# Optimization experiments

Hardware: AMD Instinct MI355X
Metric: run time of the kernel (lower is better)

## Reference

```python
import jax, jax.numpy as jnp
import numpy as np
import math

B, T, D = 2, 2048, 2048
H, DH = 16, 128
DKV, DQ, DR = 512, 1024, 64
ROPE_BASE = 500000.0
EPS = 1e-6
SCALE = 1.0 / math.sqrt(DH + DR)


def setup_inputs() -> dict:
    key = jax.random.key(0)
    ks = jax.random.split(key, 12)
    s = 0.02
    return {
        'x': jax.random.normal(ks[0], (B, T, D), jnp.float32),
        'W_DQ': jax.random.normal(ks[1], (D, DQ), jnp.float32) * s,
        'W_UQ': jax.random.normal(ks[2], (DQ, H * DH), jnp.float32) * s,
        'W_QR': jax.random.normal(ks[3], (DQ, H * DR), jnp.float32) * s,
        'W_DKV': jax.random.normal(ks[4], (D, DKV), jnp.float32) * s,
        'W_UK': jax.random.normal(ks[5], (DKV, H * DH), jnp.float32) * s,
        'W_UV': jax.random.normal(ks[6], (DKV, H * DH), jnp.float32) * s,
        'W_KR': jax.random.normal(ks[7], (D, DR), jnp.float32) * s,
        'W_O': jax.random.normal(ks[8], (H * DH, D), jnp.float32) * s,
        'q_norm_w': jnp.ones((DQ,), jnp.float32),
        'kv_norm_w': jnp.ones((DKV,), jnp.float32),
    }


def _rmsnorm(v, w):
    n = jax.lax.rsqrt(jnp.mean(v * v, axis=-1, keepdims=True) + EPS)
    return v * n * w


def _rotate_half(v):
    v1, v2 = jnp.split(v, 2, axis=-1)
    return jnp.concatenate([-v2, v1], axis=-1)


def _rope_tables(seq_len):
    inv_freq = 1.0 / (ROPE_BASE ** (jnp.arange(0, DR, 2, dtype=jnp.float32) / DR))
    t = jnp.arange(seq_len, dtype=jnp.float32)
    freqs = jnp.outer(t, inv_freq)              # (S, DR/2)
    emb = jnp.concatenate([freqs, freqs], -1)   # (S, DR)
    return jnp.cos(emb), jnp.sin(emb)


def reference(x, W_DQ, W_UQ, W_QR, W_DKV, W_UK, W_UV, W_KR, W_O, q_norm_w, kv_norm_w):
    # Query path: low-rank compress -> RMSNorm -> up-project (content + rope parts)
    c_Q = _rmsnorm(x @ W_DQ, q_norm_w)                               # (B,T,DQ)
    q_C = (c_Q @ W_UQ).reshape(B, T, H, DH).transpose(0, 2, 1, 3)    # (B,H,T,DH)
    q_R = (c_Q @ W_QR).reshape(B, T, H, DR).transpose(0, 2, 1, 3)    # (B,H,T,DR)
    # KV path: joint low-rank latent + decoupled rope key
    c_KV = _rmsnorm(x @ W_DKV, kv_norm_w)                            # (B,T,DKV)
    k_C = (c_KV @ W_UK).reshape(B, T, H, DH).transpose(0, 2, 1, 3)   # (B,H,T,DH)
    v_C = (c_KV @ W_UV).reshape(B, T, H, DH).transpose(0, 2, 1, 3)   # (B,H,T,DH)
    k_R = (x @ W_KR)[:, None, :, :]                                  # (B,1,T,DR) shared across heads
    # Decoupled RoPE
    cos, sin = _rope_tables(T)
    cos = cos[None, None]; sin = sin[None, None]                     # (1,1,T,DR)
    q_R = q_R * cos + _rotate_half(q_R) * sin
    k_R = k_R * cos + _rotate_half(k_R) * sin
    k_R = jnp.broadcast_to(k_R, (B, H, T, DR))
    q = jnp.concatenate([q_C, q_R], axis=-1)                         # (B,H,T,DH+DR)
    k = jnp.concatenate([k_C, k_R], axis=-1)
    # Causal attention with MLA scale 1/sqrt(d_head + d_rope)
    scores = jnp.einsum('bhqd,bhkd->bhqk', q, k) * SCALE
    causal = jnp.tril(jnp.ones((T, T), bool))
    scores = jnp.where(causal, scores, jnp.finfo(scores.dtype).min)
    attn = jax.nn.softmax(scores, axis=-1)
    out = jnp.einsum('bhqk,bhkd->bhqd', attn, v_C)                   # (B,H,T,DH)
    out = out.transpose(0, 2, 1, 3).reshape(B, T, H * DH)
    return out @ W_O                                                 # (B,T,D)
```

## Files before the change

kernel.cpp:

```cpp
#include <hip/hip_runtime.h>
#include <cstdint>
#include <cstddef>

#define B_   2
#define T_   2048
#define D_   2048
#define H_   16
#define DH_  128
#define DQ_  1024
#define DKV_ 512
#define DR_  64
#define M_   4096
#define SCALE_ 0.07216878364870323f
#define SC2_   0.10412808709930322f
#define LN_BASE_ 13.122363377404328f

typedef unsigned short u16;
typedef __attribute__((ext_vector_type(8))) short short8;
typedef __attribute__((ext_vector_type(4))) float f32x4;

__device__ __forceinline__ float b2f(u16 u) { return __uint_as_float(((uint32_t)u) << 16); }
__device__ __forceinline__ u16 f2b(float f) {
    uint32_t x = __float_as_uint(f);
    return (u16)((x + 0x7fffu + ((x >> 16) & 1u)) >> 16);
}
__device__ __forceinline__ u16 f2b_fast(float f) {
    return (u16)((__float_as_uint(f) + 0x8000u) >> 16);
}

struct TPack {
    const float* src[8];
    u16*         dst[8];
    int K[8];
    int N[8];
    int ntx[8];
    int start[9];
};

__global__ __launch_bounds__(256) void prep_k(TPack p, const float* __restrict__ x,
                                              u16* __restrict__ xb, int ntr) {
    const int bid = blockIdx.x;
    if (bid < ntr) {
        __shared__ float tile[32][33];
        int w = 0;
#pragma unroll
        for (int i = 1; i < 8; ++i) if (bid >= p.start[i]) w = i;
        const int lt = bid - p.start[w];
        const int bx = lt % p.ntx[w], by = lt / p.ntx[w];
        const float* in = p.src[w];
        u16* out = p.dst[w];
        const int K = p.K[w], N = p.N[w];
        const int k0 = by * 32, n0 = bx * 32;
        const int tx = threadIdx.x & 31, ty = threadIdx.x >> 5;
#pragma unroll
        for (int i = 0; i < 4; ++i) {
            int k = k0 + ty + i * 8;
            int n = n0 + tx;
            tile[ty + i * 8][tx] = (n < N) ? in[(size_t)k * N + n] : 0.f;
        }
        __syncthreads();
#pragma unroll
        for (int i = 0; i < 4; ++i) {
            int n = n0 + ty + i * 8;
            out[(size_t)n * K + k0 + tx] = f2b(tile[tx][ty + i * 8]);
        }
    } else {
        const int i = ((bid - ntr) * 256 + threadIdx.x) * 4;
        const float4 v = *(const float4*)(x + i);
        ushort4 o;
        o.x = f2b(v.x); o.y = f2b(v.y); o.z = f2b(v.z); o.w = f2b(v.w);
        *(ushort4*)(xb + i) = o;
    }
}

template <int OUT_BF16>
__global__ __launch_bounds__(256) void gemm_tn(const u16* __restrict__ A,
                                               const u16* __restrict__ Bt,
                                               void* __restrict__ Cv,
                                               int N, int K) {
    __shared__ __attribute__((aligned(16))) u16 lA[128 * 32];
    __shared__ __attribute__((aligned(16))) u16 lB[128 * 32];
    const int m0 = blockIdx.y * 128, n0 = blockIdx.x * 128;
    const int tid = threadIdx.x, wave = tid >> 6, lane = tid & 63;
    const int wm = (wave >> 1) * 64, wn = (wave & 1) * 64;
    const int r = lane & 15, kq = lane >> 4;

    f32x4 acc[4][4];
#pragma unroll
    for (int i = 0; i < 4; ++i)
#pragma unroll
        for (int j = 0; j < 4; ++j) acc[i][j] = (f32x4){0.f, 0.f, 0.f, 0.f};

    for (int kk = 0; kk < K; kk += 32) {
#pragma unroll
        for (int p = 0; p < 2; ++p) {
            const int c = p * 256 + wave * 64 + lane;
            const u16* ga = A  + (size_t)(m0 + (c >> 2)) * K + kk + (c & 3) * 8;
            const u16* gb = Bt + (size_t)(n0 + (c >> 2)) * K + kk + (c & 3) * 8;
            u16* la = lA + (size_t)(p * 256 + wave * 64) * 8;
            u16* lb = lB + (size_t)(p * 256 + wave * 64) * 8;
            __builtin_amdgcn_global_load_lds(
                (const __attribute__((address_space(1))) uint32_t*)(uintptr_t)ga,
                (__attribute__((address_space(3))) uint32_t*)(uintptr_t)la, 16, 0, 0);
            __builtin_amdgcn_global_load_lds(
                (const __attribute__((address_space(1))) uint32_t*)(uintptr_t)gb,
                (__attribute__((address_space(3))) uint32_t*)(uintptr_t)lb, 16, 0, 0);
        }
        __syncthreads();
        short8 av[4], bv[4];
#pragma unroll
        for (int mi = 0; mi < 4; ++mi)
            av[mi] = *(const short8*)&lA[(wm + mi * 16 + r) * 32 + kq * 8];
#pragma unroll
        for (int ni = 0; ni < 4; ++ni)
            bv[ni] = *(const short8*)&lB[(wn + ni * 16 + r) * 32 + kq * 8];
#pragma unroll
        for (int mi = 0; mi < 4; ++mi)
#pragma unroll
            for (int ni = 0; ni < 4; ++ni)
                acc[mi][ni] = __builtin_amdgcn_mfma_f32_16x16x32_bf16(
                    av[mi], bv[ni], acc[mi][ni], 0, 0, 0);
        __syncthreads();
    }
    const int r4 = (lane >> 4) * 4, cc = lane & 15;
#pragma unroll
    for (int mi = 0; mi < 4; ++mi)
#pragma unroll
        for (int ni = 0; ni < 4; ++ni)
#pragma unroll
            for (int i = 0; i < 4; ++i) {
                const int row = m0 + wm + mi * 16 + r4 + i;
                const int col = n0 + wn + ni * 16 + cc;
                const float v = acc[mi][ni][i];
                if (OUT_BF16) ((u16*)Cv)[(size_t)row * N + col] = f2b(v);
                else          ((float*)Cv)[(size_t)row * N + col] = v;
            }
}

__global__ __launch_bounds__(256) void gemm_pair(const u16* __restrict__ A0,
                                                 const u16* __restrict__ B0,
                                                 u16* __restrict__ C0, int N0, int K0,
                                                 const u16* __restrict__ A1,
                                                 const u16* __restrict__ B1,
                                                 u16* __restrict__ C1, int N1, int K1,
                                                 int nx0) {
    __shared__ __attribute__((aligned(16))) u16 lA[128 * 32];
    __shared__ __attribute__((aligned(16))) u16 lB[128 * 32];
    const int sel = (int)blockIdx.x >= nx0;
    const u16* A  = sel ? A1 : A0;
    const u16* Bt = sel ? B1 : B0;
    u16* Cv = sel ? C1 : C0;
    const int N = sel ? N1 : N0, K = sel ? K1 : K0;
    const int bx = sel ? (blockIdx.x - nx0) : blockIdx.x;
    const int m0 = blockIdx.y * 128, n0 = bx * 128;
    const int tid = threadIdx.x, wave = tid >> 6, lane = tid & 63;
    const int wm = (wave >> 1) * 64, wn = (wave & 1) * 64;
    const int r = lane & 15, kq = lane >> 4;

    f32x4 acc[4][4];
#pragma unroll
    for (int i = 0; i < 4; ++i)
#pragma unroll
        for (int j = 0; j < 4; ++j) acc[i][j] = (f32x4){0.f, 0.f, 0.f, 0.f};

    for (int kk = 0; kk < K; kk += 32) {
#pragma unroll
        for (int p = 0; p < 2; ++p) {
            const int c = p * 256 + wave * 64 + lane;
            const u16* ga = A  + (size_t)(m0 + (c >> 2)) * K + kk + (c & 3) * 8;
            const u16* gb = Bt + (size_t)(n0 + (c >> 2)) * K + kk + (c & 3) * 8;
            u16* la = lA + (size_t)(p * 256 + wave * 64) * 8;
            u16* lb = lB + (size_t)(p * 256 + wave * 64) * 8;
            __builtin_amdgcn_global_load_lds(
                (const __attribute__((address_space(1))) uint32_t*)(uintptr_t)ga,
                (__attribute__((address_space(3))) uint32_t*)(uintptr_t)la, 16, 0, 0);
            __builtin_amdgcn_global_load_lds(
                (const __attribute__((address_space(1))) uint32_t*)(uintptr_t)gb,
                (__attribute__((address_space(3))) uint32_t*)(uintptr_t)lb, 16, 0, 0);
        }
        __syncthreads();
        short8 av[4], bv[4];
#pragma unroll
        for (int mi = 0; mi < 4; ++mi)
            av[mi] = *(const short8*)&lA[(wm + mi * 16 + r) * 32 + kq * 8];
#pragma unroll
        for (int ni = 0; ni < 4; ++ni)
            bv[ni] = *(const short8*)&lB[(wn + ni * 16 + r) * 32 + kq * 8];
#pragma unroll
        for (int mi = 0; mi < 4; ++mi)
#pragma unroll
            for (int ni = 0; ni < 4; ++ni)
                acc[mi][ni] = __builtin_amdgcn_mfma_f32_16x16x32_bf16(
                    av[mi], bv[ni], acc[mi][ni], 0, 0, 0);
        __syncthreads();
    }
    const int r4 = (lane >> 4) * 4, cc = lane & 15;
#pragma unroll
    for (int mi = 0; mi < 4; ++mi)
#pragma unroll
        for (int ni = 0; ni < 4; ++ni)
#pragma unroll
            for (int i = 0; i < 4; ++i) {
                const int row = m0 + wm + mi * 16 + r4 + i;
                const int col = n0 + wn + ni * 16 + cc;
                Cv[(size_t)row * N + col] = f2b(acc[mi][ni][i]);
            }
}

__global__ __launch_bounds__(256) void normrope_k(const u16* __restrict__ P1,
                                                  const float* __restrict__ qnw,
                                                  const float* __restrict__ kvnw,
                                                  u16* __restrict__ cQb,
                                                  u16* __restrict__ cKVb,
                                                  u16* __restrict__ kRb) {
    const int row = blockIdx.x;
    const int which = blockIdx.y;
    if (which < 2) {
        const int N = which ? 512 : 1024;
        const int off = which ? 1024 : 0;
        const float* w = which ? kvnw : qnw;
        u16* outp = which ? cKVb : cQb;
        const u16* src = P1 + (size_t)row * 1664 + off;
        const int j = threadIdx.x * 4;
        float v[4] = {0.f, 0.f, 0.f, 0.f};
        if (j < N) {
            ushort4 u = *(const ushort4*)(src + j);
            v[0] = b2f(u.x); v[1] = b2f(u.y); v[2] = b2f(u.z); v[3] = b2f(u.w);
        }
        float ss = v[0]*v[0] + v[1]*v[1] + v[2]*v[2] + v[3]*v[3];
#pragma unroll
        for (int offc = 32; offc; offc >>= 1) ss += __shfl_down(ss, offc);
        __shared__ float red[4];
        const int wave = threadIdx.x >> 6, lane = threadIdx.x & 63;
        if (lane == 0) red[wave] = ss;
        __syncthreads();
        const float tot = red[0] + red[1] + red[2] + red[3];
        const float sc = rsqrtf(tot / (float)N + 1e-6f);
        if (j < N) {
            ushort4 o;
            o.x = f2b(v[0] * sc * w[j]);
            o.y = f2b(v[1] * sc * w[j + 1]);
            o.z = f2b(v[2] * sc * w[j + 2]);
            o.w = f2b(v[3] * sc * w[j + 3]);
            *(ushort4*)(outp + (size_t)row * N + j) = o;
        }
    } else {
        const int j = threadIdx.x;
        if (j < 64) {
            const int t = row & (T_ - 1);
            const int i = j & 31;
            const float invf = __expf(-LN_BASE_ * (float)(2 * i) * (1.0f / 64.0f));
            const float ang = (float)t * invf;
            const float c = cosf(ang), s = sinf(ang);
            const u16* src = P1 + (size_t)row * 1664 + 1536;
            const float v = b2f(src[j]);
            const float rot = (j < 32) ? -b2f(src[j + 32]) : b2f(src[j - 32]);
            kRb[(size_t)row * 64 + j] = f2b(v * c + rot * s);
        }
    }
}

__global__ __launch_bounds__(256) void epilog2_k(const u16* __restrict__ P2,
                                                 u16* __restrict__ qRb,
                                                 const u16* __restrict__ P3,
                                                 u16* __restrict__ Vt) {
    const int bid = blockIdx.x;
    if (bid < 2048) {
        const int row = bid * 2 + (threadIdx.x >> 7);
        const int t = row & (T_ - 1);
        const int e0 = (threadIdx.x & 127) * 8;
        const u16* src = P2 + (size_t)row * 3072 + 2048;
        const int j0 = e0 & 63;
        const ushort4* pv = (const ushort4*)(src + e0);
        const ushort4* pr = (const ushort4*)(src + (j0 < 32 ? e0 + 32 : e0 - 32));
        const float sgn = (j0 < 32) ? -1.f : 1.f;
        ushort4 v01 = pv[0], v23 = pv[1];
        ushort4 r01 = pr[0], r23 = pr[1];
        const u16 vv[8] = {v01.x, v01.y, v01.z, v01.w, v23.x, v23.y, v23.z, v23.w};
        const u16 rr[8] = {r01.x, r01.y, r01.z, r01.w, r23.x, r23.y, r23.z, r23.w};
        u16 o[8];
#pragma unroll
        for (int k = 0; k < 8; ++k) {
            const int i = (j0 + k) & 31;
            const float invf = __expf(-LN_BASE_ * (float)(2 * i) * (1.0f / 64.0f));
            const float ang = (float)t * invf;
            o[k] = f2b(b2f(vv[k]) * cosf(ang) + sgn * b2f(rr[k]) * sinf(ang));
        }
        *(uint4*)(qRb + (size_t)row * 1024 + e0) = *(uint4*)o;
    } else {
        __shared__ u16 tile[64][72];
        const int tt = bid - 2048;
        const int b = tt >> 10;
        const int rem = tt & 1023;
        const int by = rem >> 5, bx = rem & 31;
        const int t0 = by * 64, c0 = bx * 64;
        const int tid = threadIdx.x;
        const int rr2 = tid >> 3;
        const int c8 = tid & 7;
#pragma unroll
        for (int p = 0; p < 2; ++p) {
            const int row = p * 32 + rr2;
            *(uint4*)&tile[row][c8 * 8] =
                *(const uint4*)(P3 + (size_t)(b * T_ + t0 + row) * 4096 + 2048 + c0 + c8 * 8);
        }
        __syncthreads();
#pragma unroll
        for (int p = 0; p < 2; ++p) {
            const int c = p * 32 + rr2;
            u16 tmp[8];
#pragma unroll
            for (int j = 0; j < 8; ++j) tmp[j] = tile[c8 * 8 + j][c];
            *(uint4*)(Vt + ((size_t)b * 2048 + c0 + c) * 2048 + t0 + c8 * 8) = *(uint4*)tmp;
        }
    }
}

#define ABQ  128
#define ABK  64
#define KSTR 200
#define VSTR 72
#define PSTR 72
#define QSTRIDE 3072
#define KSTRIDE 4096

__global__ __launch_bounds__(256, 2) void attn_mfma_k(
    const u16* __restrict__ qC, const u16* __restrict__ qR,
    const u16* __restrict__ kC, const u16* __restrict__ kR,
    const u16* __restrict__ Vt, u16* __restrict__ outp)
{
    __shared__ __attribute__((aligned(16))) u16 sK[64 * KSTR];
    __shared__ __attribute__((aligned(16))) u16 sV[128 * VSTR];
    __shared__ __attribute__((aligned(16))) u16 sP[4 * 32 * PSTR];

    const int h = blockIdx.y, b = blockIdx.z;
    const int qb = b ? (15 - blockIdx.x) : blockIdx.x;
    const int q0 = qb * ABQ;
    const int tid = threadIdx.x, wave = tid >> 6, lane = tid & 63;
    const int r = lane & 15, kq = lane >> 4, r4 = kq * 4;
    const int wq = wave * 32;

    short8 qf[2][6];
#pragma unroll
    for (int mt = 0; mt < 2; ++mt) {
        const int t = q0 + wq + mt * 16 + r;
        const u16* qcrow = qC + (size_t)(b * T_ + t) * QSTRIDE + h * 128 + kq * 8;
        const u16* qrrow = qR + (size_t)(b * T_ + t) * 1024 + h * 64 + kq * 8;
#pragma unroll
        for (int kc = 0; kc < 4; ++kc) qf[mt][kc] = *(const short8*)(qcrow + kc * 32);
#pragma unroll
        for (int kc = 0; kc < 2; ++kc) qf[mt][4 + kc] = *(const short8*)(qrrow + kc * 32);
    }

    f32x4 Oa[2][8];
#pragma unroll
    for (int mt = 0; mt < 2; ++mt)
#pragma unroll
        for (int nt = 0; nt < 8; ++nt) Oa[mt][nt] = (f32x4){0.f, 0.f, 0.f, 0.f};
    float Lrow[2][4] = {{0.f,0.f,0.f,0.f},{0.f,0.f,0.f,0.f}};

    u16* myP = sP + wave * 32 * PSTR;

    const int nkt = 2 * qb + 2;
    for (int kt = 0; kt < nkt; ++kt) {
        const int k0 = kt * ABK;
        for (int i = wave; i < 25; i += 4) {
            const int s = i * 64 + lane;
            const int rr = s / 25;
            int cc = s - rr * 25;
            if (cc > 23) cc = 0;
            const int t = k0 + rr;
            const u16* src = (cc < 16)
                ? kC + (size_t)(b * T_ + t) * KSTRIDE + h * 128 + cc * 8
                : kR + (size_t)(b * T_ + t) * 64 + (cc - 16) * 8;
            __builtin_amdgcn_global_load_lds(
                (const __attribute__((address_space(1))) uint32_t*)(uintptr_t)src,
                (__attribute__((address_space(3))) uint32_t*)(uintptr_t)(sK + i * 512),
                16, 0, 0);
        }
        for (int i = wave; i < 18; i += 4) {
            const int s = i * 64 + lane;
            const int rr = s / 9;
            int cc = s - rr * 9;
            if (cc > 7) cc = 0;
            const u16* src = Vt + ((size_t)(b * H_ + h) * 128 + rr) * T_ + k0 + cc * 8;
            __builtin_amdgcn_global_load_lds(
                (const __attribute__((address_space(1))) uint32_t*)(uintptr_t)src,
                (__attribute__((address_space(3))) uint32_t*)(uintptr_t)(sV + i * 512),
                16, 0, 0);
        }
        __syncthreads();

        f32x4 Sa[2][4];
#pragma unroll
        for (int mt = 0; mt < 2; ++mt)
#pragma unroll
            for (int nt = 0; nt < 4; ++nt) Sa[mt][nt] = (f32x4){0.f, 0.f, 0.f, 0.f};
#pragma unroll
        for (int kc = 0; kc < 6; ++kc) {
            short8 kf[4];
#pragma unroll
            for (int nt = 0; nt < 4; ++nt)
                kf[nt] = *(const short8*)&sK[(nt * 16 + r) * KSTR + (kc * 4 + kq) * 8];
#pragma unroll
            for (int mt = 0; mt < 2; ++mt)
#pragma unroll
                for (int nt = 0; nt < 4; ++nt)
                    Sa[mt][nt] = __builtin_amdgcn_mfma_f32_16x16x32_bf16(
                        qf[mt][kc], kf[nt], Sa[mt][nt], 0, 0, 0);
        }

        if (kt < nkt - 2) {
#pragma unroll
            for (int mt = 0; mt < 2; ++mt)
#pragma unroll
                for (int i = 0; i < 4; ++i) {
                    float sm = 0.f;
                    float p[4];
#pragma unroll
                    for (int nt = 0; nt < 4; ++nt) {
                        p[nt] = exp2f(Sa[mt][nt][i] * SC2_);
                        sm += p[nt];
                    }
                    Lrow[mt][i] += sm;
#pragma unroll
                    for (int nt = 0; nt < 4; ++nt)
                        myP[(mt * 16 + r4 + i) * PSTR + nt * 16 + r] = f2b_fast(p[nt]);
                }
        } else {
#pragma unroll
            for (int mt = 0; mt < 2; ++mt)
#pragma unroll
                for (int i = 0; i < 4; ++i) {
                    const int grow = q0 + wq + mt * 16 + r4 + i;
                    float sm = 0.f;
                    float p[4];
#pragma unroll
                    for (int nt = 0; nt < 4; ++nt) {
                        float pv = exp2f(Sa[mt][nt][i] * SC2_);
                        p[nt] = (k0 + nt * 16 + r > grow) ? 0.f : pv;
                        sm += p[nt];
                    }
                    Lrow[mt][i] += sm;
#pragma unroll
                    for (int nt = 0; nt < 4; ++nt)
                        myP[(mt * 16 + r4 + i) * PSTR + nt * 16 + r] = f2b_fast(p[nt]);
                }
        }

#pragma unroll
        for (int kc2 = 0; kc2 < 2; ++kc2) {
            short8 pf[2];
#pragma unroll
            for (int mt = 0; mt < 2; ++mt)
                pf[mt] = *(const short8*)&myP[(mt * 16 + r) * PSTR + (kc2 * 4 + kq) * 8];
#pragma unroll
            for (int nt = 0; nt < 8; ++nt) {
                const short8 vf = *(const short8*)&sV[(nt * 16 + r) * VSTR + (kc2 * 4 + kq) * 8];
#pragma unroll
                for (int mt = 0; mt < 2; ++mt)
                    Oa[mt][nt] = __builtin_amdgcn_mfma_f32_16x16x32_bf16(
                        pf[mt], vf, Oa[mt][nt], 0, 0, 0);
            }
        }
        __syncthreads();
    }

#pragma unroll
    for (int mt = 0; mt < 2; ++mt)
#pragma unroll
        for (int i = 0; i < 4; ++i) {
            float L = Lrow[mt][i];
            L += __shfl_xor(L, 1);
            L += __shfl_xor(L, 2);
            L += __shfl_xor(L, 4);
            L += __shfl_xor(L, 8);
            const float inv = 1.0f / L;
            const int t = q0 + wq + mt * 16 + r4 + i;
            u16* orow = outp + (size_t)(b * T_ + t) * 2048 + h * 128;
#pragma unroll
            for (int nt = 0; nt < 8; ++nt)
                orow[nt * 16 + r] = f2b(Oa[mt][nt][i] * inv);
        }
}

extern "C" void kernel_launch(void* const* d_in, const int* in_sizes, int n_in,
                              void* d_out, int out_size, void* d_ws, size_t ws_size,
                              hipStream_t stream) {
    (void)in_sizes; (void)n_in; (void)out_size; (void)ws_size;
    const float* x     = (const float*)d_in[0];
    const float* W_DQ  = (const float*)d_in[1];
    const float* W_UQ  = (const float*)d_in[2];
    const float* W_QR  = (const float*)d_in[3];
    const float* W_DKV = (const float*)d_in[4];
    const float* W_UK  = (const float*)d_in[5];
    const float* W_UV  = (const float*)d_in[6];
    const float* W_KR  = (const float*)d_in[7];
    const float* W_O   = (const float*)d_in[8];
    const float* qnw   = (const float*)d_in[9];
    const float* kvnw  = (const float*)d_in[10];
    float* out = (float*)d_out;

    char* base = (char*)d_ws;
    size_t o = 0;
    auto alloc = [&](size_t bytes) {
        char* r = base + o;
        o += (bytes + 255) & ~(size_t)255;
        return r;
    };
    u16* WT1  = (u16*)alloc((size_t)1664 * 2048 * 2);
    u16* WT2  = (u16*)alloc((size_t)3072 * 1024 * 2);
    u16* WT3  = (u16*)alloc((size_t)4096 * 512 * 2);
    u16* WT_O = (u16*)alloc((size_t)2048 * 2048 * 2);
    u16* xb   = (u16*)alloc((size_t)M_ * 2048 * 2);
    u16* U1   = (u16*)alloc((size_t)M_ * 2048 * 2);
    u16* P2   = (u16*)alloc((size_t)M_ * 3072 * 2);
    u16* P3   = (u16*)alloc((size_t)M_ * 4096 * 2);
    u16* cQb  = (u16*)alloc((size_t)M_ * 1024 * 2);
    u16* cKVb = (u16*)alloc((size_t)M_ * 512 * 2);
    u16* qRb  = (u16*)alloc((size_t)M_ * 1024 * 2);
    u16* kRb  = (u16*)alloc((size_t)M_ * 64 * 2);
    u16* P1       = U1;
    u16* attn_out = U1;
    u16* Vt       = xb;

    TPack tp;
    const float* srcs[8] = {W_DQ, W_DKV, W_KR, W_UQ, W_QR, W_UK, W_UV, W_O};
    u16* dsts[8] = {WT1, WT1 + (size_t)1024*2048, WT1 + (size_t)1536*2048,
                    WT2, WT2 + (size_t)2048*1024,
                    WT3, WT3 + (size_t)2048*512, WT_O};
    const int Ks[8]   = {2048, 2048, 2048, 1024, 1024, 512, 512, 2048};
    const int Ns[8]   = {1024,  512,   64, 2048, 1024, 2048, 2048, 2048};
    const int ntxs[8] = {  32,   16,    4,   64,   32,   64,   64,   64};
    int cum = 0;
    for (int i = 0; i < 8; ++i) {
        tp.src[i] = srcs[i]; tp.dst[i] = dsts[i];
        tp.K[i] = Ks[i]; tp.N[i] = Ns[i]; tp.ntx[i] = ntxs[i];
        tp.start[i] = cum;
        cum += ntxs[i] * (Ks[i] / 32);
    }
    tp.start[8] = cum;
    const int ncast = (M_ * D_) / 1024;
    prep_k<<<cum + ncast, 256, 0, stream>>>(tp, x, xb, cum);

    gemm_tn<1><<<dim3(1664/128, M_/128), 256, 0, stream>>>(xb, WT1, (void*)P1, 1664, 2048);

    normrope_k<<<dim3(M_, 3), 256, 0, stream>>>(P1, qnw, kvnw, cQb, cKVb, kRb);

    gemm_pair<<<dim3(3072/128 + 4096/128, M_/128), 256, 0, stream>>>(
        cQb,  WT2, P2, 3072, 1024,
        cKVb, WT3, P3, 4096, 512,
        3072/128);

    epilog2_k<<<4096, 256, 0, stream>>>(P2, qRb, P3, Vt);

    attn_mfma_k<<<dim3(T_/ABQ, H_, B_), 256, 0, stream>>>(P2, qRb, P3, kRb, Vt, attn_out);

    gemm_tn<0><<<dim3(2048/128, M_/128), 256, 0, stream>>>(attn_out, WT_O, (void*)out, 2048, 2048);
}
```

Before: 441.2 us.

## Alias attention P buffer onto K tile and raise occupancy to three blocks

The separate shared-memory P buffer is removed and P is written into the K tile region after a new barrier, which lowers LDS per block. Launch bounds go from 2 to 3 blocks per CU so more blocks can be resident. The grid is also reordered so heads vary fastest, which changes block scheduling order and K/V locality. The costs are an extra __syncthreads per tile, keeping the probabilities in registers longer, and possible spills under the tighter register budget.

```diff
diff --git a/kernel.cpp b/kernel.cpp
--- a/kernel.cpp
+++ b/kernel.cpp
@@ -323,17 +323,16 @@
 #define QSTRIDE 3072
 #define KSTRIDE 4096
 
-__global__ __launch_bounds__(256, 2) void attn_mfma_k(
+__global__ __launch_bounds__(256, 3) void attn_mfma_k(
     const u16* __restrict__ qC, const u16* __restrict__ qR,
     const u16* __restrict__ kC, const u16* __restrict__ kR,
     const u16* __restrict__ Vt, u16* __restrict__ outp)
 {
     __shared__ __attribute__((aligned(16))) u16 sK[64 * KSTR];
     __shared__ __attribute__((aligned(16))) u16 sV[128 * VSTR];
-    __shared__ __attribute__((aligned(16))) u16 sP[4 * 32 * PSTR];
-
-    const int h = blockIdx.y, b = blockIdx.z;
-    const int qb = b ? (15 - blockIdx.x) : blockIdx.x;
+
+    const int h = blockIdx.x, b = blockIdx.z;
+    const int qb = b ? (15 - (int)blockIdx.y) : (int)blockIdx.y;
     const int q0 = qb * ABQ;
     const int tid = threadIdx.x, wave = tid >> 6, lane = tid & 63;
     const int r = lane & 15, kq = lane >> 4, r4 = kq * 4;
@@ -358,7 +357,7 @@
         for (int nt = 0; nt < 8; ++nt) Oa[mt][nt] = (f32x4){0.f, 0.f, 0.f, 0.f};
     float Lrow[2][4] = {{0.f,0.f,0.f,0.f},{0.f,0.f,0.f,0.f}};
 
-    u16* myP = sP + wave * 32 * PSTR;
+    u16* myP = sK + (size_t)wave * 32 * PSTR;
 
     const int nkt = 2 * qb + 2;
     for (int kt = 0; kt < nkt; ++kt) {
@@ -409,22 +408,19 @@
                         qf[mt][kc], kf[nt], Sa[mt][nt], 0, 0, 0);
         }
 
+        float pv[2][4][4];
         if (kt < nkt - 2) {
 #pragma unroll
             for (int mt = 0; mt < 2; ++mt)
 #pragma unroll
                 for (int i = 0; i < 4; ++i) {
                     float sm = 0.f;
-                    float p[4];
 #pragma unroll
                     for (int nt = 0; nt < 4; ++nt) {
-                        p[nt] = exp2f(Sa[mt][nt][i] * SC2_);
-                        sm += p[nt];
+                        pv[mt][i][nt] = exp2f(Sa[mt][nt][i] * SC2_);
+                        sm += pv[mt][i][nt];
                     }
                     Lrow[mt][i] += sm;
-#pragma unroll
-                    for (int nt = 0; nt < 4; ++nt)
-                        myP[(mt * 16 + r4 + i) * PSTR + nt * 16 + r] = f2b_fast(p[nt]);
                 }
         } else {
 #pragma unroll
@@ -433,19 +429,25 @@
                 for (int i = 0; i < 4; ++i) {
                     const int grow = q0 + wq + mt * 16 + r4 + i;
                     float sm = 0.f;
-                    float p[4];
 #pragma unroll
                     for (int nt = 0; nt < 4; ++nt) {
-                        float pv = exp2f(Sa[mt][nt][i] * SC2_);
-                        p[nt] = (k0 + nt * 16 + r > grow) ? 0.f : pv;
-                        sm += p[nt];
+                        float pvv = exp2f(Sa[mt][nt][i] * SC2_);
+                        pvv = (k0 + nt * 16 + r > grow) ? 0.f : pvv;
+                        pv[mt][i][nt] = pvv;
+                        sm += pvv;
                     }
                     Lrow[mt][i] += sm;
-#pragma unroll
-                    for (int nt = 0; nt < 4; ++nt)
-                        myP[(mt * 16 + r4 + i) * PSTR + nt * 16 + r] = f2b_fast(p[nt]);
                 }
         }
+
+        __syncthreads();
+#pragma unroll
+        for (int mt = 0; mt < 2; ++mt)
+#pragma unroll
+            for (int i = 0; i < 4; ++i)
+#pragma unroll
+                for (int nt = 0; nt < 4; ++nt)
+                    myP[(mt * 16 + r4 + i) * PSTR + nt * 16 + r] = f2b_fast(pv[mt][i][nt]);
 
 #pragma unroll
         for (int kc2 = 0; kc2 < 2; ++kc2) {
@@ -553,7 +555,7 @@
 
     epilog2_k<<<4096, 256, 0, stream>>>(P2, qRb, P3, Vt);
 
-    attn_mfma_k<<<dim3(T_/ABQ, H_, B_), 256, 0, stream>>>(P2, qRb, P3, kRb, Vt, attn_out);
+    attn_mfma_k<<<dim3(H_, T_/ABQ, B_), 256, 0, stream>>>(P2, qRb, P3, kRb, Vt, attn_out);
 
     gemm_tn<0><<<dim3(2048/128, M_/128), 256, 0, stream>>>(attn_out, WT_O, (void*)out, 2048, 2048);
 }
```

Result: slower. 578.6 us (+31.1%).
